# Optimization experiments

Hardware: AMD Instinct MI355X
Metric: run time of the kernel (lower is better)

The kernel has to match this reference:

```python
import jax, jax.numpy as jnp
import numpy as np
from jax import lax

B, H, W = 32, 80, 80
K = 100                        # max_candidates
THRESH = 0.1                   # minutiae_threshold
DIST_T = 16.0
ANGLE_T = np.pi / 6.0
PI = np.pi


def _gauss_kernel1d(ks, sigma):
    c = jnp.arange(ks, dtype=jnp.float32) - ks // 2
    g = jnp.exp(-(c * c) / (2.0 * sigma * sigma))
    return g / g.sum()


def _gaussian_blur(img):  # [B,1,H,W], separable 5x5 sigma=1.5
    k = _gauss_kernel1d(5, 1.5)
    dn = ('NCHW', 'OIHW', 'NCHW')
    x = lax.conv_general_dilated(img, k.reshape(1, 1, 1, 5), (1, 1), [(0, 0), (2, 2)], dimension_numbers=dn)
    x = lax.conv_general_dilated(x, k.reshape(1, 1, 5, 1), (1, 1), [(2, 2), (0, 0)], dimension_numbers=dn)
    return x


def _up8(m):  # nearest-neighbor x8 upsample on last two dims
    return jnp.repeat(jnp.repeat(m, 8, axis=-2), 8, axis=-1)


def _detect_and_nms(score, ori, xoff, yoff):
    # score [H,W]; ori [90,H,W]; xoff/yoff [8,H,W]
    vals, idx = lax.top_k(score.reshape(-1), K)   # sorted descending == argsort by score
    valid = vals > THRESH
    rows = idx // W
    cols = idx % W
    ang_idx = jnp.argmax(ori[:, rows, cols], axis=0)   # [K]
    xo = jnp.argmax(xoff[:, rows, cols], axis=0)
    yo = jnp.argmax(yoff[:, rows, cols], axis=0)
    angles = (ang_idx.astype(jnp.float32) * 2.0 - 89.0) * (PI / 180.0)
    x = cols.astype(jnp.float32) * 8.0 + xo.astype(jnp.float32)
    y = rows.astype(jnp.float32) * 8.0 + yo.astype(jnp.float32)
    mnt = jnp.stack([x, y, angles, vals], axis=-1)     # [K,4]
    # pairwise suppression mask (cdist + circular angle delta)
    d2 = jnp.sum((mnt[:, None, :2] - mnt[None, :, :2]) ** 2, axis=-1)
    dist = jnp.sqrt(d2)
    ad = jnp.abs(angles[:, None] - angles[None, :])
    am = jnp.minimum(ad, 2.0 * PI - ad)
    sup = (dist < DIST_T) & (am < ANGLE_T)
    ar = jnp.arange(K)
    def body(i, keep):
        s = sup[i] & (ar > i)
        return jnp.where(keep[i], keep & ~s, keep)
    keep = lax.fori_loop(0, K, body, valid)
    return mnt, keep


def setup_inputs() -> dict:
    key = jax.random.key(0)
    ks = jax.random.split(key, 7)
    return {
        'segmentation': jax.random.uniform(ks[0], (B, 1, H, W), jnp.float32),
        'minutiae_score': jax.random.uniform(ks[1], (B, 1, H, W), jnp.float32),
        'minutiae_orientation': jax.random.normal(ks[2], (B, 90, H, W), jnp.float32),
        'minutiae_x_offset': jax.random.normal(ks[3], (B, 8, H, W), jnp.float32),
        'minutiae_y_offset': jax.random.normal(ks[4], (B, 8, H, W), jnp.float32),
        'orientation': jax.random.normal(ks[5], (B, 90, H, W), jnp.float32),
        'enhanced_real': jax.random.normal(ks[6], (B, 1, 8 * H, 8 * W), jnp.float32),
    }


def reference(segmentation, minutiae_score, minutiae_orientation,
              minutiae_x_offset, minutiae_y_offset, orientation, enhanced_real):
    # --- segmentation mask: round -> gaussian blur -> round
    cleaned = jnp.round(_gaussian_blur(jnp.round(segmentation[:, 0])[:, None]))[:, 0]  # [B,H,W]
    cleaned_up = _up8(cleaned)                                                          # [B,8H,8W]
    # --- minutiae detection (threshold via masked top-k) + sequential NMS
    score = minutiae_score[:, 0] * cleaned
    mnt, keep = jax.vmap(_detect_and_nms)(score, minutiae_orientation,
                                          minutiae_x_offset, minutiae_y_offset)
    # --- orientation field
    ori_idx = jnp.argmax(orientation, axis=1).astype(jnp.float32)   # [B,H,W]
    ori_field = (_up8(ori_idx) * 2.0 - 89.0) * (PI / 180.0) * cleaned_up
    # --- enhanced image: mask + per-image min-max normalize to [0,255]
    enh = enhanced_real[:, 0] * cleaned_up
    ef = enh.reshape(B, -1)
    emin = jnp.min(ef, axis=1, keepdims=True)
    emax = jnp.max(ef, axis=1, keepdims=True)
    enorm = (ef - emin) / (emax - emin + 1e-8)
    enh_visual = enorm.reshape(B, 8 * H, 8 * W) * 255.0
    return (mnt, keep.astype(jnp.float32), enh_visual, cleaned_up * 255.0, ori_field)
```

## Files before the change

kernel.cpp:

```cpp
#include <hip/hip_runtime.h>
#include <math.h>

#define BN  32
#define H   80
#define W   80
#define HW  6400
#define KC  100
#define NCH 90
#define UW  640
#define UHW 409600

static constexpr size_t OUT_MNT   = 0;
static constexpr size_t OUT_KEEP  = (size_t)BN * KC * 4;
static constexpr size_t OUT_ENH   = OUT_KEEP + (size_t)BN * KC;
static constexpr size_t OUT_CLEAN = OUT_ENH + (size_t)BN * UHW;
static constexpr size_t OUT_ORI   = OUT_CLEAN + (size_t)BN * UHW;

#define PI_F 3.14159265358979323846
#define MM_BLOCKS 64
#define CAP 2048
#define CLEAN_BLOCKS 320
#define ORI_BLOCKS2 400
#define GAT_BLOCKS 800
#define FIN_BLOCKS 12800

typedef float vfloat4 __attribute__((ext_vector_type(4)));

__device__ __forceinline__ unsigned enc_f(float f) {
    unsigned u = __float_as_uint(f);
    return (u & 0x80000000u) ? ~u : (u | 0x80000000u);
}
__device__ __forceinline__ float dec_f(unsigned k) {
    return (k & 0x80000000u) ? __uint_as_float(k ^ 0x80000000u) : __uint_as_float(~k);
}
__device__ __forceinline__ unsigned long long shflx(unsigned long long v, int off) {
    unsigned hi = (unsigned)__shfl_xor((int)(unsigned)(v >> 32), off);
    unsigned lo = (unsigned)__shfl_xor((int)(unsigned)(v & 0xffffffffull), off);
    return ((unsigned long long)hi << 32) | lo;
}

__global__ __launch_bounds__(512) void k_pre(const float* __restrict__ seg,
                                             const float* __restrict__ ori,
                                             float* __restrict__ cleaned_g,
                                             float* __restrict__ ori_idx) {
    __shared__ __align__(16) char um[16384];
    const int bx = blockIdx.x, tid = threadIdx.x;

    if (bx < CLEAN_BLOCKS) {
        float* s_in = (float*)um;
        float* s_h  = (float*)um + 960;
        const int b = bx / 10, band = bx % 10;
        const int r0 = band * 8 - 2;

        float g[5];
        {
            float s = 0.f;
            #pragma unroll
            for (int i = 0; i < 5; i++) {
                float c = (float)(i - 2);
                g[i] = expf(-(c * c) / 4.5f);
                s += g[i];
            }
            #pragma unroll
            for (int i = 0; i < 5; i++) g[i] /= s;
        }

        for (int i = tid; i < 12 * 80; i += 512) {
            int lr = i / 80, w = i % 80;
            int gr = r0 + lr;
            s_in[i] = (gr >= 0 && gr < H) ? rintf(seg[(size_t)b * HW + gr * W + w]) : 0.f;
        }
        __syncthreads();
        for (int i = tid; i < 12 * 80; i += 512) {
            int lr = i / 80, w = i % 80;
            float acc = 0.f;
            #pragma unroll
            for (int dx = -2; dx <= 2; dx++) {
                int ww = w + dx;
                if (ww >= 0 && ww < W) acc += s_in[lr * 80 + ww] * g[dx + 2];
            }
            s_h[i] = acc;
        }
        __syncthreads();
        for (int i = tid; i < 8 * 80; i += 512) {
            int k = i / 80, w = i % 80;
            float acc = 0.f;
            #pragma unroll
            for (int dy = 0; dy < 5; dy++) acc += s_h[(k + dy) * 80 + w] * g[dy];
            cleaned_g[(size_t)b * HW + (band * 8 + k) * W + w] = rintf(acc);
        }
    } else {
        float4* s_bv = (float4*)um;
        float4* s_bj = (float4*)um + 512;
        const int grp = tid >> 7, ln = tid & 127;
        const int p4 = (bx - CLEAN_BLOCKS) * 128 + ln;
        const int b = p4 / (HW / 4), pp = p4 % (HW / 4);
        const float4* o = (const float4*)(ori + (size_t)b * NCH * HW) + pp;
        const int cs = (grp * NCH) >> 2, ce = ((grp + 1) * NCH) >> 2;

        float4 bv = o[(size_t)cs * (HW / 4)];
        float4 bj = make_float4((float)cs, (float)cs, (float)cs, (float)cs);
        for (int j = cs + 1; j < ce; j++) {
            float4 v = o[(size_t)j * (HW / 4)];
            if (v.x > bv.x) { bv.x = v.x; bj.x = (float)j; }
            if (v.y > bv.y) { bv.y = v.y; bj.y = (float)j; }
            if (v.z > bv.z) { bv.z = v.z; bj.z = (float)j; }
            if (v.w > bv.w) { bv.w = v.w; bj.w = (float)j; }
        }
        s_bv[tid] = bv; s_bj[tid] = bj;
        __syncthreads();
        if (grp == 0) {
            #pragma unroll
            for (int g = 1; g < 4; g++) {
                float4 v = s_bv[g * 128 + ln], jx = s_bj[g * 128 + ln];
                if (v.x > bv.x) { bv.x = v.x; bj.x = jx.x; }
                if (v.y > bv.y) { bv.y = v.y; bj.y = jx.y; }
                if (v.z > bv.z) { bv.z = v.z; bj.z = jx.z; }
                if (v.w > bv.w) { bv.w = v.w; bj.w = jx.w; }
            }
            ((float4*)ori_idx)[p4] = bj;
        }
    }
}

__global__ __launch_bounds__(512) void k_mid(const float* __restrict__ mscore,
                                             const float* __restrict__ cleaned,
                                             const float* __restrict__ enh,
                                             float* __restrict__ pmin,
                                             float* __restrict__ pmax,
                                             int* __restrict__ ws_idx,
                                             float* __restrict__ ws_val) {
    __shared__ __align__(16) char um[20480];
    __shared__ unsigned long long s_sel[KC];
    __shared__ unsigned s_rm[HW / 32];
    __shared__ int s_cnt[5];
    __shared__ int s_n;
    __shared__ float s_T;
    __shared__ int s_mode;
    __shared__ float smin[8], smax[8];

    const int bx = blockIdx.x, tid = threadIdx.x;
    const int lane = tid & 63;

    if (bx < BN) {
        unsigned long long* s_cand = (unsigned long long*)um;
        unsigned long long* s_red  = (unsigned long long*)um + CAP;
        const int b = bx;

        if (tid < HW / 32) s_rm[tid] = 0u;
        if (tid < 5) s_cnt[tid] = 0;
        __syncthreads();

        float sc[13];
        #pragma unroll
        for (int j = 0; j < 13; j++) {
            int i = j * 512 + tid;
            sc[j] = (i < HW) ? mscore[(size_t)b * HW + i] * cleaned[(size_t)b * HW + i]
                             : -1.0f;
        }

        int c0 = 0, c1 = 0, c2 = 0, c3 = 0, c4 = 0;
        #pragma unroll
        for (int j = 0; j < 13; j++) {
            float v = sc[j];
            c0 += (v > 0.95f); c1 += (v > 0.9f); c2 += (v > 0.8f);
            c3 += (v > 0.5f);  c4 += (v > 0.0f);
        }
        #pragma unroll
        for (int off = 32; off > 0; off >>= 1) {
            c0 += __shfl_xor(c0, off); c1 += __shfl_xor(c1, off);
            c2 += __shfl_xor(c2, off); c3 += __shfl_xor(c3, off);
            c4 += __shfl_xor(c4, off);
        }
        if (lane == 0) {
            atomicAdd(&s_cnt[0], c0); atomicAdd(&s_cnt[1], c1);
            atomicAdd(&s_cnt[2], c2); atomicAdd(&s_cnt[3], c3);
            atomicAdd(&s_cnt[4], c4);
        }
        __syncthreads();

        if (tid == 0) {
            int n95 = s_cnt[0], n90 = s_cnt[1], n80 = s_cnt[2], n50 = s_cnt[3], n0 = s_cnt[4];
            int mode; float T = 0.f;
            if (n0 < KC)                      { mode = 1; }
            else if (n95 >= KC && n95 <= CAP) { mode = 0; T = 0.95f; }
            else if (n90 >= KC && n90 <= CAP) { mode = 0; T = 0.9f; }
            else if (n80 >= KC && n80 <= CAP) { mode = 0; T = 0.8f; }
            else if (n50 >= KC && n50 <= CAP) { mode = 0; T = 0.5f; }
            else if (n0 <= CAP)               { mode = 0; T = 0.0f; }
            else                              { mode = 2; }
            s_mode = mode; s_T = T; s_n = 0;
        }
        __syncthreads();
        const int mode = s_mode;

        if (mode != 2) {
            const float T = s_T;
            #pragma unroll
            for (int j = 0; j < 13; j++) {
                int i = j * 512 + tid;
                bool take = (mode == 0) ? (sc[j] > T)
                                        : (sc[j] > 0.f || (i < 256 && sc[j] == 0.0f));
                if (take) {
                    int pos = atomicAdd(&s_n, 1);
                    s_cand[pos] = ((unsigned long long)enc_f(sc[j]) << 32) | (unsigned)(HW - i);
                }
            }
            __syncthreads();
            const int n = s_n;
            for (int c = tid; c < n; c += 512) {
                unsigned long long kk = s_cand[c];
                int rank = 0;
                for (int m = 0; m < n; m++) rank += (s_cand[m] > kk) ? 1 : 0;
                if (rank < KC) s_sel[rank] = kk;
            }
            __syncthreads();
        } else {
            for (int k = 0; k < KC; k++) {
                unsigned long long lmax = 0ull;
                #pragma unroll
                for (int j = 0; j < 13; j++) {
                    int i = j * 512 + tid;
                    if (i < HW && sc[j] >= 0.f && !((s_rm[i >> 5] >> (i & 31)) & 1u)) {
                        unsigned long long kk =
                            ((unsigned long long)enc_f(sc[j]) << 32) | (unsigned)(HW - i);
                        if (kk > lmax) lmax = kk;
                    }
                }
                s_red[tid] = lmax;
                __syncthreads();
                for (int off = 256; off > 0; off >>= 1) {
                    if (tid < off) {
                        unsigned long long o = s_red[tid + off];
                        if (o > s_red[tid]) s_red[tid] = o;
                    }
                    __syncthreads();
                }
                if (tid == 0) {
                    unsigned long long wkey = s_red[0];
                    s_sel[k] = wkey;
                    int wi = HW - (int)(wkey & 0xffffffffull);
                    s_rm[wi >> 5] |= 1u << (wi & 31);
                }
                __syncthreads();
            }
        }

        if (tid < KC) {
            unsigned long long e = s_sel[tid];
            ws_idx[(size_t)b * KC + tid] = HW - (int)(e & 0xffffffffull);
            ws_val[(size_t)b * KC + tid] = dec_f((unsigned)(e >> 32));
        }
    } else {
        const int mb = bx - BN;
        const int b = mb >> 6, chunk = mb & 63;
        const float4* e4 = (const float4*)(enh + (size_t)b * UHW);
        const float* cb = cleaned + (size_t)b * HW;

        float vmin = INFINITY, vmax = -INFINITY;
        for (int i = chunk * 512 + tid; i < UHW / 4; i += MM_BLOCKS * 512) {
            float4 v = e4[i];
            int p = i * 4;
            int Y = p / UW, X = p % UW;
            float c = cb[(Y >> 3) * W + (X >> 3)];
            float a = v.x * c, bb = v.y * c, cc = v.z * c, dd = v.w * c;
            vmin = fminf(vmin, fminf(fminf(a, bb), fminf(cc, dd)));
            vmax = fmaxf(vmax, fmaxf(fmaxf(a, bb), fmaxf(cc, dd)));
        }
        #pragma unroll
        for (int off = 32; off > 0; off >>= 1) {
            vmin = fminf(vmin, __shfl_xor(vmin, off));
            vmax = fmaxf(vmax, __shfl_xor(vmax, off));
        }
        int wave = tid >> 6;
        if (lane == 0) { smin[wave] = vmin; smax[wave] = vmax; }
        __syncthreads();
        if (tid == 0) {
            float m0 = smin[0], m1 = smax[0];
            #pragma unroll
            for (int wv = 1; wv < 8; wv++) {
                m0 = fminf(m0, smin[wv]);
                m1 = fmaxf(m1, smax[wv]);
            }
            pmin[b * MM_BLOCKS + chunk] = m0;
            pmax[b * MM_BLOCKS + chunk] = m1;
        }
    }
}

__global__ __launch_bounds__(64) void k_mm(const float* __restrict__ pmin,
                                           const float* __restrict__ pmax,
                                           float* __restrict__ mm) {
    const int b = blockIdx.x;
    float vmin = pmin[b * MM_BLOCKS + threadIdx.x];
    float vmax = pmax[b * MM_BLOCKS + threadIdx.x];
    #pragma unroll
    for (int off = 32; off > 0; off >>= 1) {
        vmin = fminf(vmin, __shfl_xor(vmin, off));
        vmax = fmaxf(vmax, __shfl_xor(vmax, off));
    }
    if (threadIdx.x == 0) { mm[2 * b] = vmin; mm[2 * b + 1] = vmax; }
}

__global__ __launch_bounds__(256) void k_fg(const float* __restrict__ enh,
                                            const float* __restrict__ cleaned,
                                            const float* __restrict__ ori_idx,
                                            const float* __restrict__ mm,
                                            const float* __restrict__ mori,
                                            const float* __restrict__ mxo,
                                            const float* __restrict__ myo,
                                            const int* __restrict__ ws_idx,
                                            const float* __restrict__ ws_val,
                                            float* __restrict__ out) {
    const int bx = blockIdx.x, tid = threadIdx.x;

    if (bx < GAT_BLOCKS) {
        const int lane = tid & 63;
        const int wid = bx * 4 + (tid >> 6);
        const int b = wid / KC, k = wid % KC;
        const int idx = ws_idx[(size_t)b * KC + k];

        const float* pm = mori + (size_t)b * NCH * HW + idx;
        unsigned long long kk =
            ((unsigned long long)enc_f(pm[(size_t)lane * HW]) << 32) | (unsigned)(127 - lane);
        if (lane < NCH - 64) {
            unsigned long long k1 =
                ((unsigned long long)enc_f(pm[(size_t)(64 + lane) * HW]) << 32)
                | (unsigned)(127 - (64 + lane));
            if (k1 > kk) kk = k1;
        }
        unsigned long long kx = 0ull, ky = 0ull;
        if (lane >= 32 && lane < 40)
            kx = ((unsigned long long)enc_f(mxo[((size_t)b * 8 + (lane - 32)) * HW + idx]) << 32)
                 | (unsigned)(15 - (lane - 32));
        if (lane >= 40 && lane < 48)
            ky = ((unsigned long long)enc_f(myo[((size_t)b * 8 + (lane - 40)) * HW + idx]) << 32)
                 | (unsigned)(15 - (lane - 40));

        #pragma unroll
        for (int off = 32; off > 0; off >>= 1) {
            unsigned long long o;
            o = shflx(kk, off); if (o > kk) kk = o;
            o = shflx(kx, off); if (o > kx) kx = o;
            o = shflx(ky, off); if (o > ky) ky = o;
        }

        if (lane == 0) {
            int ch = 127 - (int)(kk & 0xffffffffull);
            int xo = 15  - (int)(kx & 0xffffffffull);
            int yo = 15  - (int)(ky & 0xffffffffull);
            int r = idx / W, c = idx % W;
            float4 m;
            m.x = (float)c * 8.0f + (float)xo;
            m.y = (float)r * 8.0f + (float)yo;
            m.z = ((float)ch * 2.0f - 89.0f) * (float)(PI_F / 180.0);
            m.w = ws_val[(size_t)b * KC + k];
            ((float4*)(out + OUT_MNT))[(size_t)b * KC + k] = m;
        }
    } else {
        const int fb = bx - GAT_BLOCKS;
        const int b = fb / 400;
        const float emin = mm[2 * b];
        const float emax = mm[2 * b + 1];
        const float inv = 255.0f / (emax - emin + 1e-8f);

        int t4 = fb * 256 + tid;
        int p4 = t4 % (UHW / 4);
        int p = p4 * 4;
        int Y = p / UW, X = p % UW;
        int cidx = b * HW + (Y >> 3) * W + (X >> 3);
        float c  = cleaned[cidx];
        float oi = ori_idx[cidx];

        float4 e = ((const float4*)enh)[t4];
        vfloat4 ev;
        ev.x = (e.x * c - emin) * inv;
        ev.y = (e.y * c - emin) * inv;
        ev.z = (e.z * c - emin) * inv;
        ev.w = (e.w * c - emin) * inv;

        float cv = c * 255.0f;
        float ov = (oi * 2.0f - 89.0f) * (float)(PI_F / 180.0) * c;
        vfloat4 cvv = {cv, cv, cv, cv};
        vfloat4 ovv = {ov, ov, ov, ov};

        __builtin_nontemporal_store(ev,  ((vfloat4*)(out + OUT_ENH))   + t4);
        __builtin_nontemporal_store(cvv, ((vfloat4*)(out + OUT_CLEAN)) + t4);
        __builtin_nontemporal_store(ovv, ((vfloat4*)(out + OUT_ORI))   + t4);
    }
}

__global__ __launch_bounds__(64) void k_nms(float* __restrict__ out) {
    const int b = blockIdx.x, l = threadIdx.x;
    const float4* mnt = (const float4*)(out + OUT_MNT) + (size_t)b * KC;
    float4 m0 = mnt[l];
    bool has1 = (l + 64) < KC;
    float4 m1 = has1 ? mnt[l + 64] : make_float4(0.f, 0.f, 0.f, -1.f);
    int keep0 = (m0.w > 0.1f) ? 1 : 0;
    int keep1 = (has1 && m1.w > 0.1f) ? 1 : 0;

    for (int i = 0; i < KC; i++) {
        bool hi = i >= 64;
        int src = i & 63;
        float xi = __shfl(hi ? m1.x : m0.x, src);
        float yi = __shfl(hi ? m1.y : m0.y, src);
        float ai = __shfl(hi ? m1.z : m0.z, src);
        int   ki = __shfl(hi ? keep1 : keep0, src);
        if (ki) {
            if (keep0 && l > i) {
                float dx = xi - m0.x, dy = yi - m0.y;
                float dist = sqrtf(dx * dx + dy * dy);
                float ad = fabsf(ai - m0.z);
                float am = fminf(ad, (float)(2.0 * PI_F) - ad);
                if (dist < 16.0f && am < (float)(PI_F / 6.0)) keep0 = 0;
            }
            if (keep1 && (l + 64) > i) {
                float dx = xi - m1.x, dy = yi - m1.y;
                float dist = sqrtf(dx * dx + dy * dy);
                float ad = fabsf(ai - m1.z);
                float am = fminf(ad, (float)(2.0 * PI_F) - ad);
                if (dist < 16.0f && am < (float)(PI_F / 6.0)) keep1 = 0;
            }
        }
    }
    out[OUT_KEEP + (size_t)b * KC + l] = (float)keep0;
    if (has1) out[OUT_KEEP + (size_t)b * KC + 64 + l] = (float)keep1;
}

extern "C" void kernel_launch(void* const* d_in, const int* in_sizes, int n_in,
                              void* d_out, int out_size, void* d_ws, size_t ws_size,
                              hipStream_t stream) {
    const float* seg    = (const float*)d_in[0];
    const float* mscore = (const float*)d_in[1];
    const float* mori   = (const float*)d_in[2];
    const float* mxo    = (const float*)d_in[3];
    const float* myo    = (const float*)d_in[4];
    const float* ori    = (const float*)d_in[5];
    const float* enh    = (const float*)d_in[6];
    float* out = (float*)d_out;

    float* cleaned = (float*)d_ws;
    float* ori_idx = cleaned + (size_t)BN * HW;
    float* pmin    = ori_idx + (size_t)BN * HW;
    float* pmax    = pmin + (size_t)BN * MM_BLOCKS;
    float* mm      = pmax + (size_t)BN * MM_BLOCKS;
    int*   ws_idx  = (int*)(mm + 2 * BN);
    float* ws_val  = (float*)(ws_idx + (size_t)BN * KC);

    const int nPre = CLEAN_BLOCKS + ORI_BLOCKS2;
    const int nMid = BN + BN * MM_BLOCKS;
    const int nFG  = GAT_BLOCKS + FIN_BLOCKS;

    k_pre<<<nPre, 512, 0, stream>>>(seg, ori, cleaned, ori_idx);
    k_mid<<<nMid, 512, 0, stream>>>(mscore, cleaned, enh, pmin, pmax, ws_idx, ws_val);
    k_mm<<<BN, 64, 0, stream>>>(pmin, pmax, mm);
    k_fg<<<nFG, 256, 0, stream>>>(enh, cleaned, ori_idx, mm,
                                  mori, mxo, myo, ws_idx, ws_val, out);
    k_nms<<<BN, 64, 0, stream>>>(out);
}
```

Baseline: 95.65 us.

## Move cleaned and orientation-field output writes into k_mid to overlap top-k

The upsampled cleaned-mask and orientation-field stores no longer happen in the final fill kernel. They now run as extra blocks of the mid kernel, next to the per-image top-k selection and the min/max reduction. These two outputs do not depend on the global min/max, so their memory-bound writes can fill the device while the serial top-k blocks run. The final kernel then only writes the normalized enhanced image, and the mid kernel grows by 6400 blocks, which may delay the scheduling of the min/max blocks.

```diff
diff --git a/kernel.cpp b/kernel.cpp
--- a/kernel.cpp
+++ b/kernel.cpp
@@ -21,8 +21,9 @@
 #define CAP 2048
 #define CLEAN_BLOCKS 320
 #define ORI_BLOCKS2 400
+#define FINA_BLOCKS 6400
 #define GAT_BLOCKS 800
-#define FIN_BLOCKS 12800
+#define ENH_BLOCKS 12800
 
 typedef float vfloat4 __attribute__((ext_vector_type(4)));
 
@@ -126,10 +127,12 @@
 __global__ __launch_bounds__(512) void k_mid(const float* __restrict__ mscore,
                                              const float* __restrict__ cleaned,
                                              const float* __restrict__ enh,
+                                             const float* __restrict__ ori_idx,
                                              float* __restrict__ pmin,
                                              float* __restrict__ pmax,
                                              int* __restrict__ ws_idx,
-                                             float* __restrict__ ws_val) {
+                                             float* __restrict__ ws_val,
+                                             float* __restrict__ out) {
     __shared__ __align__(16) char um[20480];
     __shared__ unsigned long long s_sel[KC];
     __shared__ unsigned s_rm[HW / 32];
@@ -251,7 +254,7 @@
             ws_idx[(size_t)b * KC + tid] = HW - (int)(e & 0xffffffffull);
             ws_val[(size_t)b * KC + tid] = dec_f((unsigned)(e >> 32));
         }
-    } else {
+    } else if (bx < BN + BN * MM_BLOCKS) {
         const int mb = bx - BN;
         const int b = mb >> 6, chunk = mb & 63;
         const float4* e4 = (const float4*)(enh + (size_t)b * UHW);
@@ -285,6 +288,22 @@
             pmin[b * MM_BLOCKS + chunk] = m0;
             pmax[b * MM_BLOCKS + chunk] = m1;
         }
+    } else {
+        const int fb = bx - (BN + BN * MM_BLOCKS);
+        const int t4 = fb * 512 + tid;
+        const int b = t4 / (UHW / 4);
+        const int p4 = t4 % (UHW / 4);
+        const int p = p4 * 4;
+        const int Y = p / UW, X = p % UW;
+        const int cidx = b * HW + (Y >> 3) * W + (X >> 3);
+        const float c  = cleaned[cidx];
+        const float oi = ori_idx[cidx];
+        const float cv = c * 255.0f;
+        const float ov = (oi * 2.0f - 89.0f) * (float)(PI_F / 180.0) * c;
+        vfloat4 cvv = {cv, cv, cv, cv};
+        vfloat4 ovv = {ov, ov, ov, ov};
+        __builtin_nontemporal_store(cvv, ((vfloat4*)(out + OUT_CLEAN)) + t4);
+        __builtin_nontemporal_store(ovv, ((vfloat4*)(out + OUT_ORI))   + t4);
     }
 }
 
@@ -304,7 +323,6 @@
 
 __global__ __launch_bounds__(256) void k_fg(const float* __restrict__ enh,
                                             const float* __restrict__ cleaned,
-                                            const float* __restrict__ ori_idx,
                                             const float* __restrict__ mm,
                                             const float* __restrict__ mori,
                                             const float* __restrict__ mxo,
@@ -369,8 +387,7 @@
         int p = p4 * 4;
         int Y = p / UW, X = p % UW;
         int cidx = b * HW + (Y >> 3) * W + (X >> 3);
-        float c  = cleaned[cidx];
-        float oi = ori_idx[cidx];
+        float c = cleaned[cidx];
 
         float4 e = ((const float4*)enh)[t4];
         vfloat4 ev;
@@ -378,15 +395,7 @@
         ev.y = (e.y * c - emin) * inv;
         ev.z = (e.z * c - emin) * inv;
         ev.w = (e.w * c - emin) * inv;
-
-        float cv = c * 255.0f;
-        float ov = (oi * 2.0f - 89.0f) * (float)(PI_F / 180.0) * c;
-        vfloat4 cvv = {cv, cv, cv, cv};
-        vfloat4 ovv = {ov, ov, ov, ov};
-
-        __builtin_nontemporal_store(ev,  ((vfloat4*)(out + OUT_ENH))   + t4);
-        __builtin_nontemporal_store(cvv, ((vfloat4*)(out + OUT_CLEAN)) + t4);
-        __builtin_nontemporal_store(ovv, ((vfloat4*)(out + OUT_ORI))   + t4);
+        __builtin_nontemporal_store(ev, ((vfloat4*)(out + OUT_ENH)) + t4);
     }
 }
 
@@ -448,13 +457,14 @@
     float* ws_val  = (float*)(ws_idx + (size_t)BN * KC);
 
     const int nPre = CLEAN_BLOCKS + ORI_BLOCKS2;
-    const int nMid = BN + BN * MM_BLOCKS;
-    const int nFG  = GAT_BLOCKS + FIN_BLOCKS;
+    const int nMid = BN + BN * MM_BLOCKS + FINA_BLOCKS;
+    const int nFG  = GAT_BLOCKS + ENH_BLOCKS;
 
     k_pre<<<nPre, 512, 0, stream>>>(seg, ori, cleaned, ori_idx);
-    k_mid<<<nMid, 512, 0, stream>>>(mscore, cleaned, enh, pmin, pmax, ws_idx, ws_val);
+    k_mid<<<nMid, 512, 0, stream>>>(mscore, cleaned, enh, ori_idx,
+                                    pmin, pmax, ws_idx, ws_val, out);
     k_mm<<<BN, 64, 0, stream>>>(pmin, pmax, mm);
-    k_fg<<<nFG, 256, 0, stream>>>(enh, cleaned, ori_idx, mm,
+    k_fg<<<nFG, 256, 0, stream>>>(enh, cleaned, mm,
                                   mori, mxo, myo, ws_idx, ws_val, out);
     k_nms<<<BN, 64, 0, stream>>>(out);
 }
```

Measured after the change: 97.27 us. No clear change (+1.7%).
